# Kernel optimization log

Hardware: AMD Instinct MI355X
Metric: run time of the kernel (lower is better)

The kernel has to match this reference:

```python
import jax, jax.numpy as jnp
import numpy as np

NEG_SLOPE = 0.2
LN_EPS = 1e-5


def gat_conv(x, src, dst, n_nodes, W, a_src, a_dst, b, concat):
    # W: [F_in, H*C]; a_src, a_dst: [H, C]; b: [H*C] if concat else [C]
    H, C = a_src.shape
    h = (x @ W).reshape(-1, H, C)                      # [N, H, C]
    # per-node attention scores, gathered per edge
    s_src = jnp.einsum('nhc,hc->nh', h, a_src)          # [N, H]
    s_dst = jnp.einsum('nhc,hc->nh', h, a_dst)          # [N, H]
    e = jax.nn.leaky_relu(s_src[src] + s_dst[dst], NEG_SLOPE)  # [E, H]
    # segment softmax over incoming edges of each dst node
    e_max = jax.ops.segment_max(e, dst, num_segments=n_nodes)  # [N, H]
    w = jnp.exp(e - e_max[dst])
    denom = jax.ops.segment_sum(w, dst, num_segments=n_nodes)
    alpha = w / (denom[dst] + 1e-16)                    # [E, H]
    # weighted scatter-aggregate of source messages
    msg = h[src] * alpha[:, :, None]                    # [E, H, C]
    out = jax.ops.segment_sum(msg, dst, num_segments=n_nodes)  # [N, H, C]
    out = out.reshape(n_nodes, H * C) if concat else out.mean(axis=1)
    return out + b


def layer_norm(x, g, b):
    mu = x.mean(-1, keepdims=True)
    var = ((x - mu) ** 2).mean(-1, keepdims=True)
    return (x - mu) * jax.lax.rsqrt(var + LN_EPS) * g + b


def setup_inputs() -> dict:
    key = jax.random.key(0)
    ks = jax.random.split(key, 16)
    N, E, F_in = 50000, 400000, 128
    H1, C1 = 4, 128          # conv1: heads=4, hidden=128, concat -> 512
    C2 = 64                  # conv2: heads=1, out=64
    sd = lambda fan: 1.0 / np.sqrt(fan)
    inp = {
        'x': jax.random.normal(ks[0], (N, F_in), jnp.float32),
        'edge_index': jax.random.randint(ks[1], (2, E), 0, N, jnp.int64),
        'num_nodes': N,
        'W1': jax.random.normal(ks[2], (F_in, H1 * C1), jnp.float32) * sd(F_in),
        'a_src1': jax.random.normal(ks[3], (H1, C1), jnp.float32) * sd(C1),
        'a_dst1': jax.random.normal(ks[4], (H1, C1), jnp.float32) * sd(C1),
        'b1': jnp.zeros((H1 * C1,), jnp.float32),
        'W2': jax.random.normal(ks[5], (H1 * C1, C2), jnp.float32) * sd(H1 * C1),
        'a_src2': jax.random.normal(ks[6], (1, C2), jnp.float32) * sd(C2),
        'a_dst2': jax.random.normal(ks[7], (1, C2), jnp.float32) * sd(C2),
        'b2': jnp.zeros((C2,), jnp.float32),
        'Wm1': jax.random.normal(ks[8], (C2, 32), jnp.float32) * sd(C2),
        'bm1': jnp.zeros((32,), jnp.float32),
        'g_ln': jnp.ones((32,), jnp.float32),
        'b_ln': jnp.zeros((32,), jnp.float32),
        'Wm2': jax.random.normal(ks[9], (32, 16), jnp.float32) * sd(32),
        'bm2': jnp.zeros((16,), jnp.float32),
    }
    return inp


def reference(x, edge_index, num_nodes, W1, a_src1, a_dst1, b1, W2, a_src2, a_dst2, b2, Wm1, bm1, g_ln, b_ln, Wm2, bm2):
    N = num_nodes
    # PyG GATConv add_self_loops=True
    loop = jnp.arange(N, dtype=edge_index.dtype)
    src = jnp.concatenate([edge_index[0], loop])
    dst = jnp.concatenate([edge_index[1], loop])
    # dropout layers are identity in eval mode
    h = jax.nn.elu(gat_conv(x, src, dst, N, W1, a_src1, a_dst1, b1, concat=True))
    h = jax.nn.elu(gat_conv(h, src, dst, N, W2, a_src2, a_dst2, b2, concat=False))
    h = jax.nn.relu(layer_norm(h @ Wm1 + bm1, g_ln, b_ln))
    return h @ Wm2 + bm2  # [N, 2*n_spectral_dims]
```

## Files before the change

### kernel.cpp

```cpp
#include <hip/hip_runtime.h>
#include <cmath>


#define F_IN 128
#define H1   4
#define C1   128
#define D1   512
#define C2   64
#define DM1  32
#define DM2  16

#define LRELU(x) ((x) > 0.f ? (x) : 0.2f * (x))

typedef float f32x4 __attribute__((ext_vector_type(4)));
typedef short short8 __attribute__((ext_vector_type(8)));

static __device__ __forceinline__ float bf2f(unsigned short u) {
    return __builtin_bit_cast(float, (unsigned)u << 16);
}
static __device__ __forceinline__ unsigned short f2bf(float f) {
    unsigned u = __builtin_bit_cast(unsigned, f);
    u = (u + 0x7fffu + ((u >> 16) & 1u)) >> 16;
    return (unsigned short)u;
}

__global__ void k_detect(const void* ei, int E, int* flag) {
    __shared__ int any;
    if (threadIdx.x == 0) any = 0;
    __syncthreads();
    const int* p = (const int*)ei;
    int cnt = E < 4096 ? E : 4096;
    int stride = E / cnt;
    int local = 0;
    for (int i = threadIdx.x; i < cnt; i += blockDim.x) {
        long long idx = (long long)i * stride;
        local |= p[2 * idx + 1];
    }
    if (local) atomicOr(&any, 1);
    __syncthreads();
    if (threadIdx.x == 0) *flag = (any == 0) ? 1 : 0;
}

__global__ void k_convert(const void* ei, const int* flag, int E, int N,
                          int* src32, int* dst32, int* deg) {
    int i = blockIdx.x * blockDim.x + threadIdx.x;
    int Etot = E + N;
    if (i >= Etot) return;
    int s, d;
    if (i < E) {
        if (*flag) {
            const long long* q = (const long long*)ei;
            s = (int)q[i];
            d = (int)q[(size_t)E + i];
        } else {
            const int* q = (const int*)ei;
            s = q[i];
            d = q[(size_t)E + i];
        }
    } else {
        s = i - E;
        d = i - E;
    }
    src32[i] = s;
    dst32[i] = d;
    atomicAdd(&deg[d], 1);
}

__global__ __launch_bounds__(256) void k_scan1(const int* __restrict__ deg,
                                               int* __restrict__ bsum, int N) {
    int t = threadIdx.x;
    int base = blockIdx.x * 1024 + t * 4;
    int s = 0;
    if (base + 3 < N) {
        int4 v = *(const int4*)&deg[base];
        s = v.x + v.y + v.z + v.w;
    } else {
        for (int k = 0; k < 4; k++)
            if (base + k < N) s += deg[base + k];
    }
#pragma unroll
    for (int o = 1; o < 64; o <<= 1) s += __shfl_xor(s, o, 64);
    __shared__ int ws[4];
    if ((t & 63) == 0) ws[t >> 6] = s;
    __syncthreads();
    if (t == 0) bsum[blockIdx.x] = ws[0] + ws[1] + ws[2] + ws[3];
}

__global__ __launch_bounds__(1024) void k_scan2(const int* __restrict__ bsum,
                                                int* __restrict__ boff, int nb) {
    __shared__ int wsum[16];
    __shared__ int woff[16];
    int t = threadIdx.x, lane = t & 63, wid = t >> 6;
    int v = (t < nb) ? bsum[t] : 0;
    int x = v;
#pragma unroll
    for (int o = 1; o < 64; o <<= 1) {
        int tv = __shfl_up(x, o, 64);
        if (lane >= o) x += tv;
    }
    if (lane == 63) wsum[wid] = x;
    __syncthreads();
    if (wid == 0) {
        int y = (lane < 16) ? wsum[lane] : 0;
        int z = y;
#pragma unroll
        for (int o = 1; o < 16; o <<= 1) {
            int tv = __shfl_up(z, o, 64);
            if (lane >= o) z += tv;
        }
        if (lane < 16) woff[lane] = z - y;
    }
    __syncthreads();
    if (t < nb) boff[t] = woff[wid] + x - v;
}

__global__ __launch_bounds__(256) void k_scan3(const int* __restrict__ deg,
                                               const int* __restrict__ boff,
                                               int* __restrict__ rowstart,
                                               int* __restrict__ cursor, int N,
                                               int Etot) {
    int t = threadIdx.x, lane = t & 63, wid = t >> 6;
    int base = blockIdx.x * 1024 + t * 4;
    int v0 = 0, v1 = 0, v2 = 0, v3 = 0;
    if (base + 3 < N) {
        int4 v = *(const int4*)&deg[base];
        v0 = v.x; v1 = v.y; v2 = v.z; v3 = v.w;
    } else {
        if (base + 0 < N) v0 = deg[base + 0];
        if (base + 1 < N) v1 = deg[base + 1];
        if (base + 2 < N) v2 = deg[base + 2];
        if (base + 3 < N) v3 = deg[base + 3];
    }
    int s4 = v0 + v1 + v2 + v3;
    int x = s4;
#pragma unroll
    for (int o = 1; o < 64; o <<= 1) {
        int tv = __shfl_up(x, o, 64);
        if (lane >= o) x += tv;
    }
    __shared__ int ws[4];
    if (lane == 63) ws[wid] = x;
    __syncthreads();
    int woff = 0;
#pragma unroll
    for (int w = 0; w < 4; w++)
        if (w < wid) woff += ws[w];
    int ex = boff[blockIdx.x] + woff + (x - s4);
    int e0 = ex, e1 = ex + v0, e2 = e1 + v1, e3 = e2 + v2;
    if (base + 0 < N) { rowstart[base + 0] = e0; cursor[base + 0] = e0; }
    if (base + 1 < N) { rowstart[base + 1] = e1; cursor[base + 1] = e1; }
    if (base + 2 < N) { rowstart[base + 2] = e2; cursor[base + 2] = e2; }
    if (base + 3 < N) { rowstart[base + 3] = e3; cursor[base + 3] = e3; }
    if (blockIdx.x == 0 && t == 0) rowstart[N] = Etot;
}

__global__ void k_fill(const int* __restrict__ src32, const int* __restrict__ dst32,
                       int* __restrict__ cursor, int* __restrict__ adj, int Etot) {
    int i = blockIdx.x * blockDim.x + threadIdx.x;
    if (i < Etot) {
        int d = dst32[i];
        int pos = atomicAdd(&cursor[d], 1);
        adj[pos] = src32[i];
    }
}

__global__ void k_prep(const float* __restrict__ x, const float* __restrict__ W1,
                       const float* __restrict__ W2,
                       unsigned short* __restrict__ xb,
                       unsigned short* __restrict__ W1t,
                       unsigned short* __restrict__ W2t, int n8) {
    int i = blockIdx.x * blockDim.x + threadIdx.x;
    if (i < n8) {
        const float4* p = (const float4*)(x + (size_t)i * 8);
        float4 a = p[0], b = p[1];
        unsigned short r[8] = {f2bf(a.x), f2bf(a.y), f2bf(a.z), f2bf(a.w),
                               f2bf(b.x), f2bf(b.y), f2bf(b.z), f2bf(b.w)};
        *(short8*)(xb + (size_t)i * 8) = *(const short8*)r;
        return;
    }
    int i2 = i - n8;
    if (i2 < F_IN * D1) {
        int nn = i2 / F_IN, kk = i2 - nn * F_IN;
        W1t[i2] = f2bf(W1[(size_t)kk * D1 + nn]);
        return;
    }
    int i3 = i2 - F_IN * D1;
    if (i3 < D1 * C2) {
        int nn = i3 / D1, kk = i3 - nn * D1;
        W2t[i3] = f2bf(W2[(size_t)kk * C2 + nn]);
    }
}

template <int WM, int WN, int MF, int NF, bool OUT_BF16, int SC_MODE>
__global__ __launch_bounds__(256) void k_gemm_bf16(
    const unsigned short* __restrict__ A, const unsigned short* __restrict__ Bt,
    void* __restrict__ C, int M, int K, int NC,
    const float* __restrict__ avs, const float* __restrict__ avd,
    float* __restrict__ s_src, float* __restrict__ s_dst) {
    constexpr int BM = WM * MF * 16;
    constexpr int BN = WN * NF * 16;
    constexpr int BK = 64;
    __shared__ unsigned short As[BM * BK];
    __shared__ unsigned short Bs[BN * BK];
    __shared__ float ps_lds[WN][BM], pd_lds[WN][BM];
    const int tid = threadIdx.x;
    const int row0 = blockIdx.x * BM, col0 = blockIdx.y * BN;
    const int wave = tid >> 6, lane = tid & 63;
    const int wr = wave / WN, wc = wave % WN;
    const int lrow = lane & 15, lkg = lane >> 4;
    f32x4 acc[MF][NF] = {};
    for (int k0 = 0; k0 < K; k0 += BK) {
#pragma unroll
        for (int inst = 0; inst < (BM * 8) / 256; ++inst) {
            int ibase = inst * 256 + wave * 64;
            int i = ibase + lane;
            int r = i >> 3, u = i & 7, su = u ^ (r & 7);
            const unsigned short* gp = A + (size_t)(row0 + r) * K + k0 + su * 8;
            __builtin_amdgcn_global_load_lds(
                (const __attribute__((address_space(1))) void*)gp,
                (__attribute__((address_space(3))) void*)&As[ibase * 8], 16, 0, 0);
        }
#pragma unroll
        for (int inst = 0; inst < (BN * 8) / 256; ++inst) {
            int ibase = inst * 256 + wave * 64;
            int i = ibase + lane;
            int r = i >> 3, u = i & 7, su = u ^ (r & 7);
            const unsigned short* gp = Bt + (size_t)(col0 + r) * K + k0 + su * 8;
            __builtin_amdgcn_global_load_lds(
                (const __attribute__((address_space(1))) void*)gp,
                (__attribute__((address_space(3))) void*)&Bs[ibase * 8], 16, 0, 0);
        }
        __syncthreads();
#pragma unroll
        for (int kk = 0; kk < BK; kk += 32) {
            short8 af[MF], bfr[NF];
#pragma unroll
            for (int m = 0; m < MF; m++) {
                int ar = wr * MF * 16 + m * 16 + lrow;
                int au = kk / 8 + lkg;
                af[m] = *(const short8*)&As[(ar * 8 + (au ^ (lrow & 7))) * 8];
            }
#pragma unroll
            for (int n = 0; n < NF; n++) {
                int br = wc * NF * 16 + n * 16 + lrow;
                int au = kk / 8 + lkg;
                bfr[n] = *(const short8*)&Bs[(br * 8 + (au ^ (lrow & 7))) * 8];
            }
#pragma unroll
            for (int m = 0; m < MF; m++)
#pragma unroll
                for (int n = 0; n < NF; n++)
                    acc[m][n] = __builtin_amdgcn_mfma_f32_16x16x32_bf16(
                        af[m], bfr[n], acc[m][n], 0, 0, 0);
        }
        __syncthreads();
    }
#pragma unroll
    for (int m = 0; m < MF; m++)
#pragma unroll
        for (int n = 0; n < NF; n++)
#pragma unroll
            for (int r = 0; r < 4; r++) {
                int gr = row0 + wr * MF * 16 + m * 16 + lkg * 4 + r;
                int gc = col0 + wc * NF * 16 + n * 16 + lrow;
                if (gr < M) {
                    if (OUT_BF16)
                        ((unsigned short*)C)[(size_t)gr * NC + gc] = f2bf(acc[m][n][r]);
                    else
                        ((float*)C)[(size_t)gr * NC + gc] = acc[m][n][r];
                }
            }
    if (SC_MODE) {
        float asv[NF], adv[NF];
#pragma unroll
        for (int n = 0; n < NF; n++) {
            int gc = col0 + wc * NF * 16 + n * 16 + lrow;
            asv[n] = avs[gc];
            adv[n] = avd[gc];
        }
#pragma unroll
        for (int m = 0; m < MF; m++)
#pragma unroll
            for (int r = 0; r < 4; r++) {
                float ps = 0.f, pd = 0.f;
#pragma unroll
                for (int n = 0; n < NF; n++) {
                    ps += acc[m][n][r] * asv[n];
                    pd += acc[m][n][r] * adv[n];
                }
#pragma unroll
                for (int o = 1; o < 16; o <<= 1) {
                    ps += __shfl_xor(ps, o, 64);
                    pd += __shfl_xor(pd, o, 64);
                }
                if (lrow == 0) {
                    int lr = wr * MF * 16 + m * 16 + lkg * 4 + r;
                    ps_lds[wc][lr] = ps;
                    pd_lds[wc][lr] = pd;
                }
            }
        __syncthreads();
        for (int rr = tid; rr < BM; rr += 256) {
            int gr = row0 + rr;
            if (gr < M) {
                float s = 0.f, d = 0.f;
#pragma unroll
                for (int w = 0; w < WN; w++) {
                    s += ps_lds[w][rr];
                    d += pd_lds[w][rr];
                }
                if (SC_MODE == 1) {
                    s_src[(size_t)gr * H1 + blockIdx.y] = s;
                    s_dst[(size_t)gr * H1 + blockIdx.y] = d;
                } else {
                    s_src[gr] = s;
                    s_dst[gr] = d;
                }
            }
        }
    }
}

__global__ __launch_bounds__(256) void k_agg1(
    const unsigned short* __restrict__ h1b, const float* __restrict__ s_src,
    const float* __restrict__ s_dst, const int* __restrict__ rowstart,
    const int* __restrict__ adj, const float* __restrict__ b1,
    unsigned short* __restrict__ out1, int N) {
    int wv = (blockIdx.x * blockDim.x + threadIdx.x) >> 6;
    if (wv >= N) return;
    int lane = threadIdx.x & 63;
    int beg = rowstart[wv], end = rowstart[wv + 1];
    int h4 = lane & 3, jj = lane >> 2;
    float sdh = s_dst[(size_t)wv * 4 + h4];
    float m = -1e30f;
    for (int c0 = beg; c0 < end; c0 += 16) {
        int j = c0 + jj;
        if (j < end) {
            int sj = adj[j];
            float e = LRELU(s_src[(size_t)sj * 4 + h4] + sdh);
            m = fmaxf(m, e);
        }
    }
#pragma unroll
    for (int o = 4; o < 64; o <<= 1) m = fmaxf(m, __shfl_xor(m, o, 64));
    float dn = 0.f;
    for (int c0 = beg; c0 < end; c0 += 16) {
        int j = c0 + jj;
        if (j < end) {
            int sj = adj[j];
            float e = LRELU(s_src[(size_t)sj * 4 + h4] + sdh);
            dn += __expf(e - m);
        }
    }
#pragma unroll
    for (int o = 4; o < 64; o <<= 1) dn += __shfl_xor(dn, o, 64);
    float inv = 1.f / (dn + 1e-16f);
    int hg = lane >> 4;
    float mg = __shfl(m, hg, 64);
    float invg = __shfl(inv, hg, 64);
    float sdg = __shfl(sdh, hg, 64);
    float acc[8] = {};
    for (int j = beg; j < end; ++j) {
        int sj = adj[j];
        float e = LRELU(s_src[(size_t)sj * 4 + hg] + sdg);
        float a = __expf(e - mg) * invg;
        short8 v = *(const short8*)&h1b[(size_t)sj * D1 + lane * 8];
#pragma unroll
        for (int i = 0; i < 8; i++) acc[i] += a * bf2f((unsigned short)v[i]);
    }
    const float4* bp = (const float4*)&b1[lane * 8];
    float4 bb0 = bp[0], bb1 = bp[1];
    float r[8];
    r[0] = acc[0] + bb0.x; r[1] = acc[1] + bb0.y;
    r[2] = acc[2] + bb0.z; r[3] = acc[3] + bb0.w;
    r[4] = acc[4] + bb1.x; r[5] = acc[5] + bb1.y;
    r[6] = acc[6] + bb1.z; r[7] = acc[7] + bb1.w;
    unsigned short o16[8];
#pragma unroll
    for (int i = 0; i < 8; i++) {
        float z = r[i] > 0.f ? r[i] : expm1f(r[i]);
        o16[i] = f2bf(z);
    }
    *(short8*)&out1[(size_t)wv * D1 + lane * 8] = *(const short8*)o16;
}

__global__ __launch_bounds__(256) void k_agg2(
    const float* __restrict__ h2lin, const float* __restrict__ s_src,
    const float* __restrict__ s_dst, const int* __restrict__ rowstart,
    const int* __restrict__ adj, const float* __restrict__ b2,
    float* __restrict__ h2, int N) {
    int wv = (blockIdx.x * blockDim.x + threadIdx.x) >> 6;
    if (wv >= N) return;
    int lane = threadIdx.x & 63;
    int beg = rowstart[wv], end = rowstart[wv + 1];
    float sd = s_dst[wv];
    float m = -1e30f;
    for (int c0 = beg; c0 < end; c0 += 64) {
        int j = c0 + lane;
        if (j < end) m = fmaxf(m, LRELU(s_src[adj[j]] + sd));
    }
#pragma unroll
    for (int o = 1; o < 64; o <<= 1) m = fmaxf(m, __shfl_xor(m, o, 64));
    float dn = 0.f;
    for (int c0 = beg; c0 < end; c0 += 64) {
        int j = c0 + lane;
        if (j < end) dn += __expf(LRELU(s_src[adj[j]] + sd) - m);
    }
#pragma unroll
    for (int o = 1; o < 64; o <<= 1) dn += __shfl_xor(dn, o, 64);
    float inv = 1.f / (dn + 1e-16f);
    int eg = lane >> 4, ch = (lane & 15) * 4;
    float a0 = 0.f, a1 = 0.f, a2 = 0.f, a3 = 0.f;
    for (int j0 = beg; j0 < end; j0 += 4) {
        int j = j0 + eg;
        if (j < end) {
            int sj = adj[j];
            float a = __expf(LRELU(s_src[sj] + sd) - m) * inv;
            float4 r = *(const float4*)&h2lin[(size_t)sj * C2 + ch];
            a0 += a * r.x; a1 += a * r.y; a2 += a * r.z; a3 += a * r.w;
        }
    }
#pragma unroll
    for (int o = 16; o < 64; o <<= 1) {
        a0 += __shfl_xor(a0, o, 64);
        a1 += __shfl_xor(a1, o, 64);
        a2 += __shfl_xor(a2, o, 64);
        a3 += __shfl_xor(a3, o, 64);
    }
    if (lane < 16) {
        const float4 bb = *(const float4*)&b2[ch];
        float r0 = a0 + bb.x, r1 = a1 + bb.y, r2 = a2 + bb.z, r3 = a3 + bb.w;
        r0 = r0 > 0.f ? r0 : expm1f(r0);
        r1 = r1 > 0.f ? r1 : expm1f(r1);
        r2 = r2 > 0.f ? r2 : expm1f(r2);
        r3 = r3 > 0.f ? r3 : expm1f(r3);
        *(float4*)&h2[(size_t)wv * C2 + ch] = make_float4(r0, r1, r2, r3);
    }
}

__global__ __launch_bounds__(256) void k_mlp(
    const float* __restrict__ h2, const float* __restrict__ Wm1,
    const float* __restrict__ bm1, const float* __restrict__ g_ln,
    const float* __restrict__ b_ln, const float* __restrict__ Wm2,
    const float* __restrict__ bm2, float* __restrict__ out, int N) {
    __shared__ float w1[C2 * DM1];
    __shared__ float w2[DM1 * DM2];
    __shared__ float cb1[DM1], cg[DM1], cbl[DM1], cb2[DM2];
    int tid = threadIdx.x;
    for (int i = tid; i < C2 * DM1; i += 256) w1[i] = Wm1[i];
    for (int i = tid; i < DM1 * DM2; i += 256) w2[i] = Wm2[i];
    if (tid < DM1) {
        cb1[tid] = bm1[tid];
        cg[tid] = g_ln[tid];
        cbl[tid] = b_ln[tid];
    } else if (tid < DM1 + DM2) {
        cb2[tid - DM1] = bm2[tid - DM1];
    }
    __syncthreads();
    int n = blockIdx.x * 256 + tid;
    if (n >= N) return;
    float h[C2];
    const float4* hp = (const float4*)&h2[(size_t)n * C2];
#pragma unroll
    for (int i = 0; i < C2 / 4; i++) {
        float4 v = hp[i];
        h[4 * i] = v.x; h[4 * i + 1] = v.y;
        h[4 * i + 2] = v.z; h[4 * i + 3] = v.w;
    }
    float t[DM1];
#pragma unroll
    for (int j = 0; j < DM1; j++) {
        float a = cb1[j];
#pragma unroll
        for (int c = 0; c < C2; c++) a += h[c] * w1[c * DM1 + j];
        t[j] = a;
    }
    float mu = 0.f;
#pragma unroll
    for (int j = 0; j < DM1; j++) mu += t[j];
    mu *= (1.f / DM1);
    float var = 0.f;
#pragma unroll
    for (int j = 0; j < DM1; j++) {
        float d = t[j] - mu;
        var += d * d;
    }
    var *= (1.f / DM1);
    float rs = rsqrtf(var + 1e-5f);
#pragma unroll
    for (int j = 0; j < DM1; j++) {
        float z = (t[j] - mu) * rs * cg[j] + cbl[j];
        t[j] = z > 0.f ? z : 0.f;
    }
    float o[DM2];
#pragma unroll
    for (int k = 0; k < DM2; k++) {
        float a = cb2[k];
#pragma unroll
        for (int j = 0; j < DM1; j++) a += t[j] * w2[j * DM2 + k];
        o[k] = a;
    }
    float4* op = (float4*)&out[(size_t)n * DM2];
    op[0] = make_float4(o[0], o[1], o[2], o[3]);
    op[1] = make_float4(o[4], o[5], o[6], o[7]);
    op[2] = make_float4(o[8], o[9], o[10], o[11]);
    op[3] = make_float4(o[12], o[13], o[14], o[15]);
}

extern "C" void kernel_launch(void* const* d_in, const int* in_sizes, int n_in,
                              void* d_out, int out_size, void* d_ws,
                              size_t ws_size, hipStream_t stream) {
    const float* x      = (const float*)d_in[0];
    const void*  ei     = d_in[1];
    const float* W1     = (const float*)d_in[3];
    const float* a_src1 = (const float*)d_in[4];
    const float* a_dst1 = (const float*)d_in[5];
    const float* b1     = (const float*)d_in[6];
    const float* W2     = (const float*)d_in[7];
    const float* a_src2 = (const float*)d_in[8];
    const float* a_dst2 = (const float*)d_in[9];
    const float* b2     = (const float*)d_in[10];
    const float* Wm1    = (const float*)d_in[11];
    const float* bm1    = (const float*)d_in[12];
    const float* g_ln   = (const float*)d_in[13];
    const float* b_ln   = (const float*)d_in[14];
    const float* Wm2    = (const float*)d_in[15];
    const float* bm2    = (const float*)d_in[16];

    const int N    = in_sizes[0] / F_IN;
    const int E    = in_sizes[1] / 2;
    const int Etot = E + N;
    const int nb   = (N + 1023) / 1024;

    char* ws = (char*)d_ws;
    size_t off = 0;
    auto alloc = [&](size_t bytes) {
        size_t o = off;
        off += (bytes + 255) & ~(size_t)255;
        return o;
    };
    int*   flag     = (int*)(ws + alloc(4));
    int*   src32    = (int*)(ws + alloc((size_t)Etot * 4));
    int*   dst32    = (int*)(ws + alloc((size_t)Etot * 4));
    int*   deg      = (int*)(ws + alloc((size_t)N * 4));
    int*   bsum     = (int*)(ws + alloc(4096 * 4));
    int*   boff     = (int*)(ws + alloc(4096 * 4));
    int*   rowstart = (int*)(ws + alloc((size_t)(N + 1) * 4));
    int*   cursor   = (int*)(ws + alloc((size_t)N * 4));
    int*   adj      = (int*)(ws + alloc((size_t)Etot * 4));
    float* s_src1   = (float*)(ws + alloc((size_t)N * H1 * 4));
    float* s_dst1   = (float*)(ws + alloc((size_t)N * H1 * 4));
    unsigned short* xb   = (unsigned short*)(ws + alloc((size_t)N * F_IN * 2));
    unsigned short* W1t  = (unsigned short*)(ws + alloc((size_t)F_IN * D1 * 2));
    unsigned short* W2t  = (unsigned short*)(ws + alloc((size_t)D1 * C2 * 2));
    unsigned short* h1b  = (unsigned short*)(ws + alloc((size_t)N * D1 * 2));
    unsigned short* out1 = (unsigned short*)(ws + alloc((size_t)N * D1 * 2));
    float* h2lin = (float*)(ws + alloc((size_t)N * C2 * 4));
    float* h2    = (float*)(ws + alloc((size_t)N * C2 * 4));
    float* s_src2 = s_src1;
    float* s_dst2 = s_dst1;

    hipMemsetAsync(deg, 0, (size_t)N * 4, stream);
    k_detect<<<1, 256, 0, stream>>>(ei, E, flag);
    k_convert<<<(Etot + 255) / 256, 256, 0, stream>>>(ei, flag, E, N, src32, dst32, deg);
    k_scan1<<<nb, 256, 0, stream>>>(deg, bsum, N);
    k_scan2<<<1, 1024, 0, stream>>>(bsum, boff, nb);
    k_scan3<<<nb, 256, 0, stream>>>(deg, boff, rowstart, cursor, N, Etot);
    k_fill<<<(Etot + 255) / 256, 256, 0, stream>>>(src32, dst32, cursor, adj, Etot);

    int n8 = N * F_IN / 8;
    int prep_items = n8 + F_IN * D1 + D1 * C2;
    k_prep<<<(prep_items + 255) / 256, 256, 0, stream>>>(x, W1, W2, xb, W1t, W2t, n8);

    k_gemm_bf16<2, 2, 4, 4, true, 1>
        <<<dim3((N + 127) / 128, D1 / 128), 256, 0, stream>>>(
            xb, W1t, h1b, N, F_IN, D1, a_src1, a_dst1, s_src1, s_dst1);
    k_agg1<<<(N * 64 + 255) / 256, 256, 0, stream>>>(h1b, s_src1, s_dst1, rowstart,
                                                     adj, b1, out1, N);

    k_gemm_bf16<4, 1, 2, 4, false, 2>
        <<<dim3((N + 127) / 128, 1), 256, 0, stream>>>(
            out1, W2t, h2lin, N, D1, C2, a_src2, a_dst2, s_src2, s_dst2);
    k_agg2<<<(N * 64 + 255) / 256, 256, 0, stream>>>(h2lin, s_src2, s_dst2, rowstart,
                                                     adj, b2, h2, N);

    k_mlp<<<(N + 255) / 256, 256, 0, stream>>>(h2, Wm1, bm1, g_ln, b_ln, Wm2, bm2,
                                               (float*)d_out, N);
}
```

Measured before the change: 352.9 us.

## Fuse edge convert with prep, batch agg1 gathers, store h2lin in bf16

Merges the edge-index conversion and the bf16 prep of x and the weights into one kernel launch. Restructures the layer-1 aggregation so each 16-edge chunk computes its attention weights once in parallel, then broadcasts them by shuffle and issues four row gathers at a time. This removes the serial per-edge recomputation and exposes more memory-level parallelism. It also writes the second GEMM output as bf16 to halve gather traffic in agg2, at the cost of extra precision loss.

```diff
diff --git a/kernel.cpp b/kernel.cpp
--- a/kernel.cpp
+++ b/kernel.cpp
@@ -22,6 +22,12 @@
     unsigned u = __builtin_bit_cast(unsigned, f);
     u = (u + 0x7fffu + ((u >> 16) & 1u)) >> 16;
     return (unsigned short)u;
+}
+static __device__ __forceinline__ float bflo(unsigned d) {
+    return __builtin_bit_cast(float, d << 16);
+}
+static __device__ __forceinline__ float bfhi(unsigned d) {
+    return __builtin_bit_cast(float, d & 0xffff0000u);
 }
 
 __global__ void k_detect(const void* ei, int E, int* flag) {
@@ -41,29 +47,57 @@
     if (threadIdx.x == 0) *flag = (any == 0) ? 1 : 0;
 }
 
-__global__ void k_convert(const void* ei, const int* flag, int E, int N,
-                          int* src32, int* dst32, int* deg) {
+__global__ void k_convert_prep(const void* ei, const int* flag, int E, int N,
+                               int* src32, int* dst32, int* deg,
+                               const float* __restrict__ x,
+                               const float* __restrict__ W1,
+                               const float* __restrict__ W2,
+                               unsigned short* __restrict__ xb,
+                               unsigned short* __restrict__ W1t,
+                               unsigned short* __restrict__ W2t, int n8) {
     int i = blockIdx.x * blockDim.x + threadIdx.x;
     int Etot = E + N;
-    if (i >= Etot) return;
-    int s, d;
-    if (i < E) {
-        if (*flag) {
-            const long long* q = (const long long*)ei;
-            s = (int)q[i];
-            d = (int)q[(size_t)E + i];
+    if (i < Etot) {
+        int s, d;
+        if (i < E) {
+            if (*flag) {
+                const long long* q = (const long long*)ei;
+                s = (int)q[i];
+                d = (int)q[(size_t)E + i];
+            } else {
+                const int* q = (const int*)ei;
+                s = q[i];
+                d = q[(size_t)E + i];
+            }
         } else {
-            const int* q = (const int*)ei;
-            s = q[i];
-            d = q[(size_t)E + i];
-        }
-    } else {
-        s = i - E;
-        d = i - E;
-    }
-    src32[i] = s;
-    dst32[i] = d;
-    atomicAdd(&deg[d], 1);
+            s = i - E;
+            d = i - E;
+        }
+        src32[i] = s;
+        dst32[i] = d;
+        atomicAdd(&deg[d], 1);
+        return;
+    }
+    int i1 = i - Etot;
+    if (i1 < n8) {
+        const float4* p = (const float4*)(x + (size_t)i1 * 8);
+        float4 a = p[0], b = p[1];
+        unsigned short r[8] = {f2bf(a.x), f2bf(a.y), f2bf(a.z), f2bf(a.w),
+                               f2bf(b.x), f2bf(b.y), f2bf(b.z), f2bf(b.w)};
+        *(short8*)(xb + (size_t)i1 * 8) = *(const short8*)r;
+        return;
+    }
+    int i2 = i1 - n8;
+    if (i2 < F_IN * D1) {
+        int nn = i2 / F_IN, kk = i2 - nn * F_IN;
+        W1t[i2] = f2bf(W1[(size_t)kk * D1 + nn]);
+        return;
+    }
+    int i3 = i2 - F_IN * D1;
+    if (i3 < D1 * C2) {
+        int nn = i3 / D1, kk = i3 - nn * D1;
+        W2t[i3] = f2bf(W2[(size_t)kk * C2 + nn]);
+    }
 }
 
 __global__ __launch_bounds__(256) void k_scan1(const int* __restrict__ deg,
@@ -161,33 +195,6 @@
         int d = dst32[i];
         int pos = atomicAdd(&cursor[d], 1);
         adj[pos] = src32[i];
-    }
-}
-
-__global__ void k_prep(const float* __restrict__ x, const float* __restrict__ W1,
-                       const float* __restrict__ W2,
-                       unsigned short* __restrict__ xb,
-                       unsigned short* __restrict__ W1t,
-                       unsigned short* __restrict__ W2t, int n8) {
-    int i = blockIdx.x * blockDim.x + threadIdx.x;
-    if (i < n8) {
-        const float4* p = (const float4*)(x + (size_t)i * 8);
-        float4 a = p[0], b = p[1];
-        unsigned short r[8] = {f2bf(a.x), f2bf(a.y), f2bf(a.z), f2bf(a.w),
-                               f2bf(b.x), f2bf(b.y), f2bf(b.z), f2bf(b.w)};
-        *(short8*)(xb + (size_t)i * 8) = *(const short8*)r;
-        return;
-    }
-    int i2 = i - n8;
-    if (i2 < F_IN * D1) {
-        int nn = i2 / F_IN, kk = i2 - nn * F_IN;
-        W1t[i2] = f2bf(W1[(size_t)kk * D1 + nn]);
-        return;
-    }
-    int i3 = i2 - F_IN * D1;
-    if (i3 < D1 * C2) {
-        int nn = i3 / D1, kk = i3 - nn * D1;
-        W2t[i3] = f2bf(W2[(size_t)kk * C2 + nn]);
     }
 }
 
@@ -356,25 +363,54 @@
     for (int o = 4; o < 64; o <<= 1) dn += __shfl_xor(dn, o, 64);
     float inv = 1.f / (dn + 1e-16f);
     int hg = lane >> 4;
-    float mg = __shfl(m, hg, 64);
-    float invg = __shfl(inv, hg, 64);
-    float sdg = __shfl(sdh, hg, 64);
-    float acc[8] = {};
-    for (int j = beg; j < end; ++j) {
-        int sj = adj[j];
-        float e = LRELU(s_src[(size_t)sj * 4 + hg] + sdg);
-        float a = __expf(e - mg) * invg;
-        short8 v = *(const short8*)&h1b[(size_t)sj * D1 + lane * 8];
-#pragma unroll
-        for (int i = 0; i < 8; i++) acc[i] += a * bf2f((unsigned short)v[i]);
-    }
+    float aL[4] = {}, aH[4] = {};
+#define ACC1(vv, aa)                                   \
+    do {                                               \
+        aL[0] += (aa)*bflo(vv.x); aH[0] += (aa)*bfhi(vv.x); \
+        aL[1] += (aa)*bflo(vv.y); aH[1] += (aa)*bfhi(vv.y); \
+        aL[2] += (aa)*bflo(vv.z); aH[2] += (aa)*bfhi(vv.z); \
+        aL[3] += (aa)*bflo(vv.w); aH[3] += (aa)*bfhi(vv.w); \
+    } while (0)
+    for (int c0 = beg; c0 < end; c0 += 16) {
+        int j = c0 + jj;
+        float av = 0.f;
+        int sjv = 0;
+        if (j < end) {
+            sjv = adj[j];
+            float e = LRELU(s_src[(size_t)sjv * 4 + h4] + sdh);
+            av = __expf(e - m) * inv;
+        }
+        int cnt = min(16, end - c0);
+        int j2 = 0;
+        for (; j2 + 4 <= cnt; j2 += 4) {
+            int l0 = (j2 + 0) * 4 + hg, l1 = (j2 + 1) * 4 + hg;
+            int l2 = (j2 + 2) * 4 + hg, l3 = (j2 + 3) * 4 + hg;
+            int s0 = __shfl(sjv, l0, 64), s1 = __shfl(sjv, l1, 64);
+            int s2 = __shfl(sjv, l2, 64), s3 = __shfl(sjv, l3, 64);
+            float a0 = __shfl(av, l0, 64), a1 = __shfl(av, l1, 64);
+            float a2 = __shfl(av, l2, 64), a3 = __shfl(av, l3, 64);
+            uint4 v0 = *(const uint4*)&h1b[(size_t)s0 * D1 + lane * 8];
+            uint4 v1 = *(const uint4*)&h1b[(size_t)s1 * D1 + lane * 8];
+            uint4 v2 = *(const uint4*)&h1b[(size_t)s2 * D1 + lane * 8];
+            uint4 v3 = *(const uint4*)&h1b[(size_t)s3 * D1 + lane * 8];
+            ACC1(v0, a0); ACC1(v1, a1); ACC1(v2, a2); ACC1(v3, a3);
+        }
+        for (; j2 < cnt; ++j2) {
+            int l0 = j2 * 4 + hg;
+            int s0 = __shfl(sjv, l0, 64);
+            float a0 = __shfl(av, l0, 64);
+            uint4 v0 = *(const uint4*)&h1b[(size_t)s0 * D1 + lane * 8];
+            ACC1(v0, a0);
+        }
+    }
+#undef ACC1
     const float4* bp = (const float4*)&b1[lane * 8];
     float4 bb0 = bp[0], bb1 = bp[1];
     float r[8];
-    r[0] = acc[0] + bb0.x; r[1] = acc[1] + bb0.y;
-    r[2] = acc[2] + bb0.z; r[3] = acc[3] + bb0.w;
-    r[4] = acc[4] + bb1.x; r[5] = acc[5] + bb1.y;
-    r[6] = acc[6] + bb1.z; r[7] = acc[7] + bb1.w;
+    r[0] = aL[0] + bb0.x; r[1] = aH[0] + bb0.y;
+    r[2] = aL[1] + bb0.z; r[3] = aH[1] + bb0.w;
+    r[4] = aL[2] + bb1.x; r[5] = aH[2] + bb1.y;
+    r[6] = aL[3] + bb1.z; r[7] = aH[3] + bb1.w;
     unsigned short o16[8];
 #pragma unroll
     for (int i = 0; i < 8; i++) {
@@ -385,7 +421,7 @@
 }
 
 __global__ __launch_bounds__(256) void k_agg2(
-    const float* __restrict__ h2lin, const float* __restrict__ s_src,
+    const unsigned short* __restrict__ h2lin, const float* __restrict__ s_src,
     const float* __restrict__ s_dst, const int* __restrict__ rowstart,
     const int* __restrict__ adj, const float* __restrict__ b2,
     float* __restrict__ h2, int N) {
@@ -416,8 +452,9 @@
         if (j < end) {
             int sj = adj[j];
             float a = __expf(LRELU(s_src[sj] + sd) - m) * inv;
-            float4 r = *(const float4*)&h2lin[(size_t)sj * C2 + ch];
-            a0 += a * r.x; a1 += a * r.y; a2 += a * r.z; a3 += a * r.w;
+            uint2 rv = *(const uint2*)&h2lin[(size_t)sj * C2 + ch];
+            a0 += a * bflo(rv.x); a1 += a * bfhi(rv.x);
+            a2 += a * bflo(rv.y); a3 += a * bfhi(rv.y);
         }
     }
 #pragma unroll
@@ -550,27 +587,26 @@
     int*   adj      = (int*)(ws + alloc((size_t)Etot * 4));
     float* s_src1   = (float*)(ws + alloc((size_t)N * H1 * 4));
     float* s_dst1   = (float*)(ws + alloc((size_t)N * H1 * 4));
-    unsigned short* xb   = (unsigned short*)(ws + alloc((size_t)N * F_IN * 2));
-    unsigned short* W1t  = (unsigned short*)(ws + alloc((size_t)F_IN * D1 * 2));
-    unsigned short* W2t  = (unsigned short*)(ws + alloc((size_t)D1 * C2 * 2));
-    unsigned short* h1b  = (unsigned short*)(ws + alloc((size_t)N * D1 * 2));
-    unsigned short* out1 = (unsigned short*)(ws + alloc((size_t)N * D1 * 2));
-    float* h2lin = (float*)(ws + alloc((size_t)N * C2 * 4));
+    unsigned short* xb    = (unsigned short*)(ws + alloc((size_t)N * F_IN * 2));
+    unsigned short* W1t   = (unsigned short*)(ws + alloc((size_t)F_IN * D1 * 2));
+    unsigned short* W2t   = (unsigned short*)(ws + alloc((size_t)D1 * C2 * 2));
+    unsigned short* h1b   = (unsigned short*)(ws + alloc((size_t)N * D1 * 2));
+    unsigned short* out1  = (unsigned short*)(ws + alloc((size_t)N * D1 * 2));
+    unsigned short* h2lin = (unsigned short*)(ws + alloc((size_t)N * C2 * 2));
     float* h2    = (float*)(ws + alloc((size_t)N * C2 * 4));
     float* s_src2 = s_src1;
     float* s_dst2 = s_dst1;
 
     hipMemsetAsync(deg, 0, (size_t)N * 4, stream);
     k_detect<<<1, 256, 0, stream>>>(ei, E, flag);
-    k_convert<<<(Etot + 255) / 256, 256, 0, stream>>>(ei, flag, E, N, src32, dst32, deg);
+    int n8 = N * F_IN / 8;
+    int total_cp = Etot + n8 + F_IN * D1 + D1 * C2;
+    k_convert_prep<<<(total_cp + 255) / 256, 256, 0, stream>>>(
+        ei, flag, E, N, src32, dst32, deg, x, W1, W2, xb, W1t, W2t, n8);
     k_scan1<<<nb, 256, 0, stream>>>(deg, bsum, N);
     k_scan2<<<1, 1024, 0, stream>>>(bsum, boff, nb);
     k_scan3<<<nb, 256, 0, stream>>>(deg, boff, rowstart, cursor, N, Etot);
     k_fill<<<(Etot + 255) / 256, 256, 0, stream>>>(src32, dst32, cursor, adj, Etot);
-
-    int n8 = N * F_IN / 8;
-    int prep_items = n8 + F_IN * D1 + D1 * C2;
-    k_prep<<<(prep_items + 255) / 256, 256, 0, stream>>>(x, W1, W2, xb, W1t, W2t, n8);
 
     k_gemm_bf16<2, 2, 4, 4, true, 1>
         <<<dim3((N + 127) / 128, D1 / 128), 256, 0, stream>>>(
@@ -578,7 +614,7 @@
     k_agg1<<<(N * 64 + 255) / 256, 256, 0, stream>>>(h1b, s_src1, s_dst1, rowstart,
                                                      adj, b1, out1, N);
 
-    k_gemm_bf16<4, 1, 2, 4, false, 2>
+    k_gemm_bf16<4, 1, 2, 4, true, 2>
         <<<dim3((N + 127) / 128, 1), 256, 0, stream>>>(
             out1, W2t, h2lin, N, D1, C2, a_src2, a_dst2, s_src2, s_dst2);
     k_agg2<<<(N * 64 + 255) / 256, 256, 0, stream>>>(h2lin, s_src2, s_dst2, rowstart,
```

New measurement: 340.9 us. -3.4%, faster.
